# Performance work log

Hardware: AMD Instinct MI355X
Metric: run time of the kernel (lower is better)

## Reference

```python
import jax, jax.numpy as jnp
import numpy as np

G, B, K, D = 16384, 4, 2, 64
NEG = -1e30


def _mlp3(x, w1, b1, w2, b2, w3, b3):
    # MLP: linear->relu x3 (BatchNorm defined but unused in original forward)
    h = jax.nn.relu(x @ w1 + b1)
    h = jax.nn.relu(h @ w2 + b2)
    return jax.nn.relu(h @ w3 + b3)


def setup_inputs() -> dict:
    key = jax.random.key(0)
    ks = jax.random.split(key, 32)

    def lin(k, fan_in, fan_out):
        k1, k2 = jax.random.split(k)
        s = 1.0 / np.sqrt(fan_in)
        w = jax.random.uniform(k1, (fan_in, fan_out), jnp.float32, -s, s)
        b = jax.random.uniform(k2, (fan_out,), jnp.float32, -s, s)
        return w, b

    inp = {}
    inp['ap_feat'] = jax.random.normal(ks[0], (G, B, 1), jnp.float32)
    inp['e_feat'] = jax.random.normal(ks[1], (G, B, K, 2), jnp.float32)
    inp['w_pre_ap'], inp['b_pre_ap'] = lin(ks[2], 1, D)
    inp['w_pre_edge'], inp['b_pre_edge'] = lin(ks[3], 2, D)
    # mlp_update_5 (AP-side neighbor messages), _6 (UE-side), _7 (edge update)
    inp['w5_1'], inp['b5_1'] = lin(ks[4], 2 * D, D)
    inp['w5_2'], inp['b5_2'] = lin(ks[5], D, D)
    inp['w5_3'], inp['b5_3'] = lin(ks[6], D, D)
    inp['w6_1'], inp['b6_1'] = lin(ks[7], 2 * D, D)
    inp['w6_2'], inp['b6_2'] = lin(ks[8], D, D)
    inp['w6_3'], inp['b6_3'] = lin(ks[9], D, D)
    inp['w7_1'], inp['b7_1'] = lin(ks[10], 2 * D, D)
    inp['w7_2'], inp['b7_2'] = lin(ks[11], D, D)
    inp['w7_3'], inp['b7_3'] = lin(ks[12], D, D)
    inp['w_post'], inp['b_post'] = lin(ks[13], D, 2)
    return inp


def _edge_conv(e, a, w5_1, b5_1, w5_2, b5_2, w5_3, b5_3,
               w6_1, b6_1, w6_2, b6_2, w6_3, b6_3,
               w7_1, b7_1, w7_2, b7_2, w7_3, b7_3):
    # e: [G,B,K,D] AP2UE edge hid; a: [G,B,D] AP hid.
    # M1[g,b,j] = mlp5(cat(a[g,b], e[g,b,j])) -- same-AP neighbor edges
    x1 = jnp.concatenate([jnp.broadcast_to(a[:, :, None, :], e.shape), e], axis=-1)  # [G,B,K,2D]
    M1 = _mlp3(x1, w5_1, b5_1, w5_2, b5_2, w5_3, b5_3)  # [G,B,K,D]
    # M2[g,b,bp,k] = mlp6(cat(a[g,b], e[g,bp,k])) -- same-UE neighbor edges
    # (original uses the SRC AP feature here too). Split first linear to
    # avoid materializing the [G,B,B,K,2D] concat.
    h = jax.nn.relu(
        (a @ w6_1[:D])[:, :, None, None, :]
        + (e @ w6_1[D:])[:, None, :, :, :]
        + b6_1)  # [G,B,B,K,D]
    h = jax.nn.relu(h @ w6_2 + b6_2)
    M2 = jax.nn.relu(h @ w6_3 + b6_3)  # [G,B,Bp,K,D]
    # masked max excluding the edge itself
    eyeK = jnp.eye(K, dtype=bool)  # [k, j]
    m1max = jnp.max(jnp.where(eyeK[None, None, :, :, None], NEG,
                              M1[:, :, None, :, :]), axis=3)  # [G,B,K,D]
    eyeB = jnp.eye(B, dtype=bool)  # [b, bp]
    m2max = jnp.max(jnp.where(eyeB[None, :, :, None, None], NEG, M2), axis=2)  # [G,B,K,D]
    agg = jnp.maximum(m1max, m2max)
    # new edge feature: mlp7(cat(agg, e_hid))
    return _mlp3(jnp.concatenate([agg, e], axis=-1),
                 w7_1, b7_1, w7_2, b7_2, w7_3, b7_3)


def reference(ap_feat, e_feat, w_pre_ap, b_pre_ap, w_pre_edge, b_pre_edge,
              w5_1, b5_1, w5_2, b5_2, w5_3, b5_3,
              w6_1, b6_1, w6_2, b6_2, w6_3, b6_3,
              w7_1, b7_1, w7_2, b7_2, w7_3, b7_3,
              w_post, b_post):
    # PreLayer (live branches only: AP nodes and AP2UE edges; APConv/UEConv
    # write node 'new' which is never read, so UE/UE2AP branches are dead).
    a = jax.nn.relu(ap_feat @ w_pre_ap + b_pre_ap)   # [G,B,D]
    e = jax.nn.relu(e_feat @ w_pre_edge + b_pre_edge)  # [G,B,K,D]
    # two UpdateLayers (shared weights: ModuleList([UpdateLayer()]*2) + global MLPs)
    for _ in range(2):
        e = _edge_conv(e, a, w5_1, b5_1, w5_2, b5_2, w5_3, b5_3,
                       w6_1, b6_1, w6_2, b6_2, w6_3, b6_3,
                       w7_1, b7_1, w7_2, b7_2, w7_3, b7_3)
    out = e @ w_post + b_post  # [G,B,K,2]
    r, im = out[..., 0], out[..., 1]
    # norm_func: per-graph [B,K] complex matrix, each row (over K) L2-normalized
    n = jnp.sqrt(jnp.sum(r * r + im * im, axis=-1, keepdims=True))
    return jnp.stack([r / n, im / n], axis=-1)  # [G,B,K,2]
```

## Files before the change

### kernel.cpp

```cpp
#include <hip/hip_runtime.h>


typedef unsigned short u16;
typedef unsigned int   u32;
typedef __attribute__((ext_vector_type(8))) short short8_t;
typedef __attribute__((ext_vector_type(2))) short short2v;
typedef __attribute__((ext_vector_type(4))) float floatx4;

#define OFF_W51 0
#define OFF_W61 8192
#define OFF_W71 16384
#define OFF_W52 24576
#define OFF_W53 28672
#define OFF_W62 32768
#define OFF_W63 36864
#define OFF_W72 40960
#define OFF_W73 45056
#define WS_U16  49152

#define CB51 0
#define CB52 64
#define CB53 128
#define CB61 192
#define CB62 256
#define CB63 320
#define CB71 384
#define CB72 448
#define CB73 512
#define CWPO 576
#define CBPO 704
#define CWPA 768
#define CBPA 832
#define CWPE 896
#define CBPE 1024
#define CSZ  1088

#define PW_U16 3584

struct Params {
  const float *ap, *ef;
  const float *wpa, *bpa, *wpe, *bpe;
  const float *w51, *b51, *w52, *b52, *w53, *b53;
  const float *w61, *b61, *w62, *b62, *w63, *b63;
  const float *w71, *b71, *w72, *b72, *w73, *b73;
  const float *wpost, *bpost;
  float *out;
  int gtot;
};

__device__ __forceinline__ u32 pk2(float a, float b) {
  const u32 ua = __float_as_uint(a) + 0x8000u;
  const u32 ub = __float_as_uint(b) + 0x8000u;
  return __builtin_amdgcn_perm(ub, ua, 0x07060302u);
}
__device__ __forceinline__ float blo(u32 v) { return __uint_as_float(v << 16); }
__device__ __forceinline__ float bhi(u32 v) { return __uint_as_float(v & 0xffff0000u); }
__device__ __forceinline__ u32 pkmax(u32 a, u32 b) {
  const short2v r = __builtin_elementwise_max(__builtin_bit_cast(short2v, a),
                                              __builtin_bit_cast(short2v, b));
  return __builtin_bit_cast(u32, r);
}
__device__ __forceinline__ u32 ror16(u32 x) { return (x >> 16) | (x << 16); }
__device__ __forceinline__ float sel4(int i, float x0, float x1, float x2, float x3) {
  const float lo = (i & 1) ? x1 : x0;
  const float hi = (i & 1) ? x3 : x2;
  return (i & 2) ? hi : lo;
}

__device__ __forceinline__ floatx4 mfma16(short8_t a, short8_t b, floatx4 c) {
  return __builtin_amdgcn_mfma_f32_16x16x32_bf16(a, b, c, 0, 0, 0);
}
__device__ __forceinline__ short8_t ldA(const u16* buf, int l) {
  return *(const short8_t*)(buf + l * 8);
}

template<int TSTRIDE>
__device__ __forceinline__ void layerK64R(floatx4* acc, short8_t a0, short8_t a1,
                                          const u16* B, int l) {
#pragma unroll
  for (int t = 0; t < 4; ++t) {
    const short8_t b0 = *(const short8_t*)(B + (t * TSTRIDE + 0) * 512 + l * 8);
    const short8_t b1 = *(const short8_t*)(B + (t * TSTRIDE + 1) * 512 + l * 8);
    acc[t] = mfma16(a0, b0, acc[t]);
    acc[t] = mfma16(a1, b1, acc[t]);
  }
}

__device__ __forceinline__ void layerK64B(floatx4* acc, short8_t a0, short8_t a1,
                                          const short8_t* Bw) {
#pragma unroll
  for (int t = 0; t < 4; ++t) {
    acc[t] = mfma16(a0, Bw[2 * t + 0], acc[t]);
    acc[t] = mfma16(a1, Bw[2 * t + 1], acc[t]);
  }
}

__device__ __forceinline__ void layerK128R(floatx4* acc, short8_t a0, short8_t a1,
                                           short8_t a2, short8_t a3,
                                           const u16* B, int l) {
  short8_t a[4] = {a0, a1, a2, a3};
#pragma unroll
  for (int t = 0; t < 4; ++t)
#pragma unroll
    for (int h = 0; h < 4; ++h)
      acc[t] = mfma16(a[h], *(const short8_t*)(B + (t * 4 + h) * 512 + l * 8), acc[t]);
}

__device__ __forceinline__ void scatter_relu_bf16(u16* dst, const floatx4* acc, int q, int n) {
#pragma unroll
  for (int t = 0; t < 4; ++t) {
    const int kk = (t & 1) * 2 + (n >> 3);
    u16* base = dst + (t >> 1) * 512 + (n & 7);
    const u32 v01 = pk2(fmaxf(acc[t][0], 0.f), fmaxf(acc[t][1], 0.f));
    const u32 v23 = pk2(fmaxf(acc[t][2], 0.f), fmaxf(acc[t][3], 0.f));
    base[(4 * q + 0 + 16 * kk) * 8] = (u16)v01;
    base[(4 * q + 1 + 16 * kk) * 8] = (u16)(v01 >> 16);
    base[(4 * q + 2 + 16 * kk) * 8] = (u16)v23;
    base[(4 * q + 3 + 16 * kk) * 8] = (u16)(v23 >> 16);
  }
}

__device__ __forceinline__ void scatter_bf16(u16* dst, const floatx4* acc, int q, int n) {
#pragma unroll
  for (int t = 0; t < 4; ++t) {
    const int kk = (t & 1) * 2 + (n >> 3);
    u16* base = dst + (t >> 1) * 512 + (n & 7);
    const u32 v01 = pk2(acc[t][0], acc[t][1]);
    const u32 v23 = pk2(acc[t][2], acc[t][3]);
    base[(4 * q + 0 + 16 * kk) * 8] = (u16)v01;
    base[(4 * q + 1 + 16 * kk) * 8] = (u16)(v01 >> 16);
    base[(4 * q + 2 + 16 * kk) * 8] = (u16)v23;
    base[(4 * q + 3 + 16 * kk) * 8] = (u16)(v23 >> 16);
  }
}

__device__ __forceinline__ void scatter_pk(u16* dst, const u32* src, int q, int n) {
#pragma unroll
  for (int t = 0; t < 4; ++t) {
    const int kk = (t & 1) * 2 + (n >> 3);
    u16* base = dst + (t >> 1) * 512 + (n & 7);
#pragma unroll
    for (int half = 0; half < 2; ++half) {
      const u32 v = src[2 * t + half];
      base[(4 * q + 2 * half + 0 + 16 * kk) * 8] = (u16)v;
      base[(4 * q + 2 * half + 1 + 16 * kk) * 8] = (u16)(v >> 16);
    }
  }
}

__device__ __forceinline__ void scatter_aP(u16* dst, const floatx4* acc, int q, int n,
                                           const float* cb61) {
#pragma unroll
  for (int t = 0; t < 4; ++t) {
    const int kk = (t & 1) * 2 + (n >> 3);
    u16* base = dst + (t >> 1) * 256 + (n & 7);
    const float bv = cb61[16 * t + n];
    const u32 v = pk2(acc[t][0] + bv, acc[t][2] + bv);
    base[(2 * q + 0 + 8 * kk) * 8] = (u16)v;
    base[(2 * q + 1 + 8 * kk) * 8] = (u16)(v >> 16);
  }
}

__device__ __forceinline__ void init_accL(floatx4* acc, const float* cb, int n) {
#pragma unroll
  for (int t = 0; t < 4; ++t) {
    const float b = cb[16 * t + n];
    floatx4 v; v[0] = b; v[1] = b; v[2] = b; v[3] = b;
    acc[t] = v;
  }
}

struct frag2 { short8_t f0, f1; };

__device__ __forceinline__ frag2 make_a(float apv, int q, const float* sc) {
  frag2 r;
#pragma unroll
  for (int h = 0; h < 2; ++h) {
    const int fb = 32 * h + 8 * q;
    const float4 wa0 = *(const float4*)(sc + CWPA + fb);
    const float4 wa1 = *(const float4*)(sc + CWPA + fb + 4);
    const float4 ba0 = *(const float4*)(sc + CBPA + fb);
    const float4 ba1 = *(const float4*)(sc + CBPA + fb + 4);
    uint4 pa;
    pa.x = pk2(fmaxf(fmaf(apv, wa0.x, ba0.x), 0.f), fmaxf(fmaf(apv, wa0.y, ba0.y), 0.f));
    pa.y = pk2(fmaxf(fmaf(apv, wa0.z, ba0.z), 0.f), fmaxf(fmaf(apv, wa0.w, ba0.w), 0.f));
    pa.z = pk2(fmaxf(fmaf(apv, wa1.x, ba1.x), 0.f), fmaxf(fmaf(apv, wa1.y, ba1.y), 0.f));
    pa.w = pk2(fmaxf(fmaf(apv, wa1.z, ba1.z), 0.f), fmaxf(fmaf(apv, wa1.w, ba1.w), 0.f));
    if (h == 0) r.f0 = __builtin_bit_cast(short8_t, pa);
    else        r.f1 = __builtin_bit_cast(short8_t, pa);
  }
  return r;
}

#define NBLK 256
#define NWAVE 8
#define PPW  4

__global__ __launch_bounds__(512)
__attribute__((amdgpu_waves_per_eu(2)))
void hetgnn_mfma(Params p) {
  __shared__ __align__(16) u16   sW[WS_U16];
  __shared__ __align__(16) u16   sAct[NWAVE * PW_U16];
  __shared__ __align__(16) float sConst[CSZ];

  const int tid  = threadIdx.x;
  const int wave = tid >> 6;
  const int l    = tid & 63;
  const int q    = l >> 4;
  const int n    = l & 15;

  {
    const float* mats[9] = {p.w51, p.w61, p.w71, p.w52, p.w53, p.w62, p.w63, p.w72, p.w73};
    for (int i = 0; i < 12; ++i) {
      const int fi = wave * 12 + i;
      const float* W;
      int t, h;
      if (fi < 48) { W = mats[fi >> 4]; const int loc = fi & 15; t = loc >> 2; h = loc & 3; }
      else { const int j = fi - 48; W = mats[3 + (j >> 3)]; const int loc = j & 7; t = loc >> 1; h = loc & 1; }
      const int nn = 16 * t + (l & 15);
      const int k0 = 32 * h + (l >> 4) * 8;
      float w[8];
#pragma unroll
      for (int j = 0; j < 8; ++j) w[j] = W[(k0 + j) * 64 + nn];
      uint4 o;
      o.x = pk2(w[0], w[1]); o.y = pk2(w[2], w[3]);
      o.z = pk2(w[4], w[5]); o.w = pk2(w[6], w[7]);
      *(uint4*)(sW + fi * 512 + l * 8) = o;
    }
  }
  if (tid < 64) {
    sConst[CB51 + tid] = p.b51[tid];
    sConst[CB52 + tid] = p.b52[tid];
    sConst[CB53 + tid] = p.b53[tid];
    sConst[CB61 + tid] = p.b61[tid];
    sConst[CB62 + tid] = p.b62[tid];
    sConst[CB63 + tid] = p.b63[tid];
    sConst[CB71 + tid] = p.b71[tid];
    sConst[CB72 + tid] = p.b72[tid];
    sConst[CB73 + tid] = p.b73[tid];
    sConst[CWPA + tid] = p.wpa[tid];
    sConst[CBPA + tid] = p.bpa[tid];
    sConst[CBPE + tid] = p.bpe[tid];
  }
  if (tid < 128) {
    sConst[CWPO + tid] = p.wpost[tid];
    sConst[CWPE + tid] = p.wpe[tid];
  }
  if (tid < 2) sConst[CBPO + tid] = p.bpost[tid];
  __syncthreads();

  short8_t bw62[8], bw63[8];
#pragma unroll
  for (int f = 0; f < 8; ++f) {
    bw62[f] = *(const short8_t*)(sW + OFF_W62 + f * 512 + l * 8);
    bw63[f] = *(const short8_t*)(sW + OFF_W63 + f * 512 + l * 8);
  }

  u16* Eb  = sAct + wave * PW_U16;
  u16* T1  = Eb + 1024;
  u16* eP  = Eb + 2048;
  u16* aPb = Eb + 3072;

  const int wslot = blockIdx.x * NWAVE + wave;

  for (int pi = 0; pi < PPW; ++pi) {
    const int g0 = (wslot * PPW + pi) * 2;
    if (g0 + 2 > p.gtot) break;

    const float apv = p.ap[(g0 + (n >> 3)) * 4 + ((n >> 1) & 3)];
    const frag2 A = make_a(apv, q, sConst);
    short8_t e0, e1;
    {
      const float f0 = p.ef[(g0 + (n >> 3)) * 16 + (n & 7) * 2];
      const float f1 = p.ef[(g0 + (n >> 3)) * 16 + (n & 7) * 2 + 1];
#pragma unroll
      for (int h = 0; h < 2; ++h) {
        const int fb = 32 * h + 8 * q;
        const float4 w00 = *(const float4*)(sConst + CWPE + fb);
        const float4 w01 = *(const float4*)(sConst + CWPE + fb + 4);
        const float4 w10 = *(const float4*)(sConst + CWPE + 64 + fb);
        const float4 w11 = *(const float4*)(sConst + CWPE + 64 + fb + 4);
        const float4 be0 = *(const float4*)(sConst + CBPE + fb);
        const float4 be1 = *(const float4*)(sConst + CBPE + fb + 4);
        uint4 pe;
        pe.x = pk2(fmaxf(fmaf(f0, w00.x, fmaf(f1, w10.x, be0.x)), 0.f),
                   fmaxf(fmaf(f0, w00.y, fmaf(f1, w10.y, be0.y)), 0.f));
        pe.y = pk2(fmaxf(fmaf(f0, w00.z, fmaf(f1, w10.z, be0.z)), 0.f),
                   fmaxf(fmaf(f0, w00.w, fmaf(f1, w10.w, be0.w)), 0.f));
        pe.z = pk2(fmaxf(fmaf(f0, w01.x, fmaf(f1, w11.x, be1.x)), 0.f),
                   fmaxf(fmaf(f0, w01.y, fmaf(f1, w11.y, be1.y)), 0.f));
        pe.w = pk2(fmaxf(fmaf(f0, w01.z, fmaf(f1, w11.z, be1.z)), 0.f),
                   fmaxf(fmaf(f0, w01.w, fmaf(f1, w11.w, be1.w)), 0.f));
        if (h == 0) e0 = __builtin_bit_cast(short8_t, pe);
        else        e1 = __builtin_bit_cast(short8_t, pe);
      }
    }

    {
      floatx4 accA[4];
#pragma unroll
      for (int t = 0; t < 4; ++t) { accA[t][0] = 0.f; accA[t][1] = 0.f; accA[t][2] = 0.f; accA[t][3] = 0.f; }
      layerK64R<4>(accA, A.f0, A.f1, sW + OFF_W61, l);
      scatter_aP(aPb, accA, q, n, sConst + CB61);
    }

#pragma unroll 1
    for (int it = 0; it < 2; ++it) {
      if (it == 1) { e0 = ldA(Eb, l); e1 = ldA(Eb + 512, l); }

      u32 m1p[8];
      {
        floatx4 acc[4]; init_accL(acc, sConst + CB51, n);
        layerK128R(acc, A.f0, A.f1, e0, e1, sW + OFF_W51, l);
        scatter_relu_bf16(T1, acc, q, n);
        floatx4 acc2[4]; init_accL(acc2, sConst + CB52, n);
        layerK64R<2>(acc2, ldA(T1, l), ldA(T1 + 512, l), sW + OFF_W52, l);
        scatter_relu_bf16(T1, acc2, q, n);
        floatx4 acc3[4]; init_accL(acc3, sConst + CB53, n);
        layerK64R<2>(acc3, ldA(T1, l), ldA(T1 + 512, l), sW + OFF_W53, l);
#pragma unroll
        for (int t = 0; t < 4; ++t) {
          m1p[2 * t + 0] = pk2(acc3[t][0], acc3[t][1]);
          m1p[2 * t + 1] = pk2(acc3[t][2], acc3[t][3]);
        }
      }

      u32 m2p[8];
      {
        floatx4 accE[4];
#pragma unroll
        for (int t = 0; t < 4; ++t) { accE[t][0] = 0.f; accE[t][1] = 0.f; accE[t][2] = 0.f; accE[t][3] = 0.f; }
        layerK64R<4>(accE, e0, e1, sW + OFF_W61 + 2 * 512, l);
        scatter_bf16(eP, accE, q, n);

        const int d = n >> 1;
        const int b_ln = (n >> 1) & 3;
#pragma unroll
        for (int j = 0; j < 3; ++j) {
          const int bp = (j >= b_ln) ? (j + 1) : j;
          const int re = (n & 8) + bp * 2 + (n & 1);
          short8_t h0, h1;
#pragma unroll
          for (int h = 0; h < 2; ++h) {
            const uint4 av = *(const uint4*)(aPb + h * 256 + (d + 8 * q) * 8);
            const uint4 ev = *(const uint4*)(eP + h * 512 + (re + 16 * q) * 8);
            uint4 ph;
            ph.x = pk2(fmaxf(blo(av.x) + blo(ev.x), 0.f),
                       fmaxf(bhi(av.x) + bhi(ev.x), 0.f));
            ph.y = pk2(fmaxf(blo(av.y) + blo(ev.y), 0.f),
                       fmaxf(bhi(av.y) + bhi(ev.y), 0.f));
            ph.z = pk2(fmaxf(blo(av.z) + blo(ev.z), 0.f),
                       fmaxf(bhi(av.z) + bhi(ev.z), 0.f));
            ph.w = pk2(fmaxf(blo(av.w) + blo(ev.w), 0.f),
                       fmaxf(bhi(av.w) + bhi(ev.w), 0.f));
            if (h == 0) h0 = __builtin_bit_cast(short8_t, ph);
            else        h1 = __builtin_bit_cast(short8_t, ph);
          }
          floatx4 acc2[4]; init_accL(acc2, sConst + CB62, n);
          layerK64B(acc2, h0, h1, bw62);
          scatter_relu_bf16(T1, acc2, q, n);
          floatx4 acc3[4]; init_accL(acc3, sConst + CB63, n);
          layerK64B(acc3, ldA(T1, l), ldA(T1 + 512, l), bw63);
#pragma unroll
          for (int t = 0; t < 4; ++t) {
#pragma unroll
            for (int h = 0; h < 2; ++h) {
              const u32 cand = pk2(acc3[t][2 * h], acc3[t][2 * h + 1]);
              m2p[2 * t + h] = (j == 0) ? cand : pkmax(m2p[2 * t + h], cand);
            }
          }
        }
      }

      {
        u32 agp[8];
#pragma unroll
        for (int i = 0; i < 8; ++i)
          agp[i] = pkmax(pkmax(ror16(m1p[i]), m2p[i]), 0u);
        scatter_pk(T1, agp, q, n);
        floatx4 acc[4]; init_accL(acc, sConst + CB71, n);
        layerK128R(acc, ldA(T1, l), ldA(T1 + 512, l), e0, e1, sW + OFF_W71, l);
        scatter_relu_bf16(T1, acc, q, n);
        floatx4 acc2[4]; init_accL(acc2, sConst + CB72, n);
        layerK64R<2>(acc2, ldA(T1, l), ldA(T1 + 512, l), sW + OFF_W72, l);
        scatter_relu_bf16(T1, acc2, q, n);
        floatx4 acc3[4]; init_accL(acc3, sConst + CB73, n);
        layerK64R<2>(acc3, ldA(T1, l), ldA(T1 + 512, l), sW + OFF_W73, l);

        if (it == 0) {
          scatter_relu_bf16(Eb, acc3, q, n);
        } else {
          float prr[4] = {0.f, 0.f, 0.f, 0.f}, pii[4] = {0.f, 0.f, 0.f, 0.f};
#pragma unroll
          for (int t = 0; t < 4; ++t) {
            const float wr = sConst[CWPO + (16 * t + n) * 2];
            const float wi = sConst[CWPO + (16 * t + n) * 2 + 1];
#pragma unroll
            for (int r = 0; r < 4; ++r) {
              const float e = fmaxf(acc3[t][r], 0.f);
              prr[r] = fmaf(e, wr, prr[r]);
              pii[r] = fmaf(e, wi, pii[r]);
            }
          }
          const float bpR = sConst[CBPO], bpI = sConst[CBPO + 1];
#pragma unroll
          for (int r = 0; r < 4; ++r) {
#pragma unroll
            for (int off = 1; off < 16; off <<= 1) {
              prr[r] += __shfl_xor(prr[r], off, 16);
              pii[r] += __shfl_xor(pii[r], off, 16);
            }
            prr[r] += bpR;
            pii[r] += bpI;
          }
          const int r = n >> 1, c = n & 1, rp = r ^ 1;
          const float pr_r  = sel4(r,  prr[0], prr[1], prr[2], prr[3]);
          const float pi_r  = sel4(r,  pii[0], pii[1], pii[2], pii[3]);
          const float pr_rp = sel4(rp, prr[0], prr[1], prr[2], prr[3]);
          const float pi_rp = sel4(rp, pii[0], pii[1], pii[2], pii[3]);
          const float num = c ? pi_r : pr_r;
          const float n2  = pr_r * pr_r + pi_r * pi_r + pr_rp * pr_rp + pi_rp * pi_rp;
          if (n < 8) p.out[g0 * 16 + (4 * q + r) * 2 + c] = num / sqrtf(n2);
        }
      }
    }
  }
}

extern "C" void kernel_launch(void* const* d_in, const int* in_sizes, int n_in,
                              void* d_out, int out_size, void* d_ws, size_t ws_size,
                              hipStream_t stream) {
  Params p;
  p.ap    = (const float*)d_in[0];
  p.ef    = (const float*)d_in[1];
  p.wpa   = (const float*)d_in[2];  p.bpa   = (const float*)d_in[3];
  p.wpe   = (const float*)d_in[4];  p.bpe   = (const float*)d_in[5];
  p.w51   = (const float*)d_in[6];  p.b51   = (const float*)d_in[7];
  p.w52   = (const float*)d_in[8];  p.b52   = (const float*)d_in[9];
  p.w53   = (const float*)d_in[10]; p.b53   = (const float*)d_in[11];
  p.w61   = (const float*)d_in[12]; p.b61   = (const float*)d_in[13];
  p.w62   = (const float*)d_in[14]; p.b62   = (const float*)d_in[15];
  p.w63   = (const float*)d_in[16]; p.b63   = (const float*)d_in[17];
  p.w71   = (const float*)d_in[18]; p.b71   = (const float*)d_in[19];
  p.w72   = (const float*)d_in[20]; p.b72   = (const float*)d_in[21];
  p.w73   = (const float*)d_in[22]; p.b73   = (const float*)d_in[23];
  p.wpost = (const float*)d_in[24]; p.bpost = (const float*)d_in[25];
  p.out   = (float*)d_out;
  p.gtot  = in_sizes[0] / 4;

  hipLaunchKernelGGL(hetgnn_mfma, dim3(NBLK), dim3(512), 0, stream, p);
}
```

Measured before the change: 166.0 us.

## Double waves per block by shrinking per-wave LDS and register footprint

Raises each block from 8 to 16 waves (1024 threads, waves_per_eu 4) and halves the pairs handled per wave. To make room, the four per-wave activation buffers are collapsed into one shared scratch plus the aP buffer. The W62 weight fragments are now built straight from global memory into registers, while W63 is no longer held in registers and is read from LDS instead. The M2 hidden fragments are precomputed for all three neighbours before the MLP passes, since the scratch buffer that held eP is later overwritten. This trades extra LDS reads and register pressure limits for higher occupancy and latency hiding.

```diff
diff --git a/kernel.cpp b/kernel.cpp
--- a/kernel.cpp
+++ b/kernel.cpp
@@ -12,11 +12,10 @@
 #define OFF_W71 16384
 #define OFF_W52 24576
 #define OFF_W53 28672
-#define OFF_W62 32768
-#define OFF_W63 36864
-#define OFF_W72 40960
-#define OFF_W73 45056
-#define WS_U16  49152
+#define OFF_W63 32768
+#define OFF_W72 36864
+#define OFF_W73 40960
+#define WS_U16  45056
 
 #define CB51 0
 #define CB52 64
@@ -35,7 +34,7 @@
 #define CBPE 1024
 #define CSZ  1088
 
-#define PW_U16 3584
+#define PW_U16 1536
 
 struct Params {
   const float *ap, *ef;
@@ -193,11 +192,11 @@
 }
 
 #define NBLK 256
-#define NWAVE 8
-#define PPW  4
-
-__global__ __launch_bounds__(512)
-__attribute__((amdgpu_waves_per_eu(2)))
+#define NWAVE 16
+#define PPW  2
+
+__global__ __launch_bounds__(1024)
+__attribute__((amdgpu_waves_per_eu(4)))
 void hetgnn_mfma(Params p) {
   __shared__ __align__(16) u16   sW[WS_U16];
   __shared__ __align__(16) u16   sAct[NWAVE * PW_U16];
@@ -210,15 +209,14 @@
   const int n    = l & 15;
 
   {
-    const float* mats[9] = {p.w51, p.w61, p.w71, p.w52, p.w53, p.w62, p.w63, p.w72, p.w73};
-    for (int i = 0; i < 12; ++i) {
-      const int fi = wave * 12 + i;
+    const float* mats[8] = {p.w51, p.w61, p.w71, p.w52, p.w53, p.w63, p.w72, p.w73};
+    for (int fi = wave; fi < 88; fi += NWAVE) {
       const float* W;
       int t, h;
       if (fi < 48) { W = mats[fi >> 4]; const int loc = fi & 15; t = loc >> 2; h = loc & 3; }
       else { const int j = fi - 48; W = mats[3 + (j >> 3)]; const int loc = j & 7; t = loc >> 1; h = loc & 1; }
-      const int nn = 16 * t + (l & 15);
-      const int k0 = 32 * h + (l >> 4) * 8;
+      const int nn = 16 * t + n;
+      const int k0 = 32 * h + q * 8;
       float w[8];
 #pragma unroll
       for (int j = 0; j < 8; ++j) w[j] = W[(k0 + j) * 64 + nn];
@@ -249,17 +247,22 @@
   if (tid < 2) sConst[CBPO + tid] = p.bpost[tid];
   __syncthreads();
 
-  short8_t bw62[8], bw63[8];
+  short8_t bw62[8];
 #pragma unroll
   for (int f = 0; f < 8; ++f) {
-    bw62[f] = *(const short8_t*)(sW + OFF_W62 + f * 512 + l * 8);
-    bw63[f] = *(const short8_t*)(sW + OFF_W63 + f * 512 + l * 8);
-  }
-
-  u16* Eb  = sAct + wave * PW_U16;
-  u16* T1  = Eb + 1024;
-  u16* eP  = Eb + 2048;
-  u16* aPb = Eb + 3072;
+    const int nn = 16 * (f >> 1) + n;
+    const int k0 = 32 * (f & 1) + q * 8;
+    float w[8];
+#pragma unroll
+    for (int j = 0; j < 8; ++j) w[j] = p.w62[(k0 + j) * 64 + nn];
+    uint4 o;
+    o.x = pk2(w[0], w[1]); o.y = pk2(w[2], w[3]);
+    o.z = pk2(w[4], w[5]); o.w = pk2(w[6], w[7]);
+    bw62[f] = __builtin_bit_cast(short8_t, o);
+  }
+
+  u16* BUF = sAct + wave * PW_U16;
+  u16* aPb = BUF + 1024;
 
   const int wslot = blockIdx.x * NWAVE + wave;
 
@@ -306,18 +309,18 @@
 
 #pragma unroll 1
     for (int it = 0; it < 2; ++it) {
-      if (it == 1) { e0 = ldA(Eb, l); e1 = ldA(Eb + 512, l); }
+      if (it == 1) { e0 = ldA(BUF, l); e1 = ldA(BUF + 512, l); }
 
       u32 m1p[8];
       {
         floatx4 acc[4]; init_accL(acc, sConst + CB51, n);
         layerK128R(acc, A.f0, A.f1, e0, e1, sW + OFF_W51, l);
-        scatter_relu_bf16(T1, acc, q, n);
+        scatter_relu_bf16(BUF, acc, q, n);
         floatx4 acc2[4]; init_accL(acc2, sConst + CB52, n);
-        layerK64R<2>(acc2, ldA(T1, l), ldA(T1 + 512, l), sW + OFF_W52, l);
-        scatter_relu_bf16(T1, acc2, q, n);
+        layerK64R<2>(acc2, ldA(BUF, l), ldA(BUF + 512, l), sW + OFF_W52, l);
+        scatter_relu_bf16(BUF, acc2, q, n);
         floatx4 acc3[4]; init_accL(acc3, sConst + CB53, n);
-        layerK64R<2>(acc3, ldA(T1, l), ldA(T1 + 512, l), sW + OFF_W53, l);
+        layerK64R<2>(acc3, ldA(BUF, l), ldA(BUF + 512, l), sW + OFF_W53, l);
 #pragma unroll
         for (int t = 0; t < 4; ++t) {
           m1p[2 * t + 0] = pk2(acc3[t][0], acc3[t][1]);
@@ -331,19 +334,19 @@
 #pragma unroll
         for (int t = 0; t < 4; ++t) { accE[t][0] = 0.f; accE[t][1] = 0.f; accE[t][2] = 0.f; accE[t][3] = 0.f; }
         layerK64R<4>(accE, e0, e1, sW + OFF_W61 + 2 * 512, l);
-        scatter_bf16(eP, accE, q, n);
+        scatter_bf16(BUF, accE, q, n);
 
         const int d = n >> 1;
-        const int b_ln = (n >> 1) & 3;
+        const int b_ln = d & 3;
+        short8_t hf0[3], hf1[3];
 #pragma unroll
         for (int j = 0; j < 3; ++j) {
           const int bp = (j >= b_ln) ? (j + 1) : j;
           const int re = (n & 8) + bp * 2 + (n & 1);
-          short8_t h0, h1;
 #pragma unroll
           for (int h = 0; h < 2; ++h) {
             const uint4 av = *(const uint4*)(aPb + h * 256 + (d + 8 * q) * 8);
-            const uint4 ev = *(const uint4*)(eP + h * 512 + (re + 16 * q) * 8);
+            const uint4 ev = *(const uint4*)(BUF + h * 512 + (re + 16 * q) * 8);
             uint4 ph;
             ph.x = pk2(fmaxf(blo(av.x) + blo(ev.x), 0.f),
                        fmaxf(bhi(av.x) + bhi(ev.x), 0.f));
@@ -353,14 +356,17 @@
                        fmaxf(bhi(av.z) + bhi(ev.z), 0.f));
             ph.w = pk2(fmaxf(blo(av.w) + blo(ev.w), 0.f),
                        fmaxf(bhi(av.w) + bhi(ev.w), 0.f));
-            if (h == 0) h0 = __builtin_bit_cast(short8_t, ph);
-            else        h1 = __builtin_bit_cast(short8_t, ph);
+            if (h == 0) hf0[j] = __builtin_bit_cast(short8_t, ph);
+            else        hf1[j] = __builtin_bit_cast(short8_t, ph);
           }
+        }
+#pragma unroll
+        for (int j = 0; j < 3; ++j) {
           floatx4 acc2[4]; init_accL(acc2, sConst + CB62, n);
-          layerK64B(acc2, h0, h1, bw62);
-          scatter_relu_bf16(T1, acc2, q, n);
+          layerK64B(acc2, hf0[j], hf1[j], bw62);
+          scatter_relu_bf16(BUF, acc2, q, n);
           floatx4 acc3[4]; init_accL(acc3, sConst + CB63, n);
-          layerK64B(acc3, ldA(T1, l), ldA(T1 + 512, l), bw63);
+          layerK64R<2>(acc3, ldA(BUF, l), ldA(BUF + 512, l), sW + OFF_W63, l);
 #pragma unroll
           for (int t = 0; t < 4; ++t) {
 #pragma unroll
@@ -377,18 +383,18 @@
 #pragma unroll
         for (int i = 0; i < 8; ++i)
           agp[i] = pkmax(pkmax(ror16(m1p[i]), m2p[i]), 0u);
-        scatter_pk(T1, agp, q, n);
+        scatter_pk(BUF, agp, q, n);
         floatx4 acc[4]; init_accL(acc, sConst + CB71, n);
-        layerK128R(acc, ldA(T1, l), ldA(T1 + 512, l), e0, e1, sW + OFF_W71, l);
-        scatter_relu_bf16(T1, acc, q, n);
+        layerK128R(acc, ldA(BUF, l), ldA(BUF + 512, l), e0, e1, sW + OFF_W71, l);
+        scatter_relu_bf16(BUF, acc, q, n);
         floatx4 acc2[4]; init_accL(acc2, sConst + CB72, n);
-        layerK64R<2>(acc2, ldA(T1, l), ldA(T1 + 512, l), sW + OFF_W72, l);
-        scatter_relu_bf16(T1, acc2, q, n);
+        layerK64R<2>(acc2, ldA(BUF, l), ldA(BUF + 512, l), sW + OFF_W72, l);
+        scatter_relu_bf16(BUF, acc2, q, n);
         floatx4 acc3[4]; init_accL(acc3, sConst + CB73, n);
-        layerK64R<2>(acc3, ldA(T1, l), ldA(T1 + 512, l), sW + OFF_W73, l);
+        layerK64R<2>(acc3, ldA(BUF, l), ldA(BUF + 512, l), sW + OFF_W73, l);
 
         if (it == 0) {
-          scatter_relu_bf16(Eb, acc3, q, n);
+          scatter_relu_bf16(BUF, acc3, q, n);
         } else {
           float prr[4] = {0.f, 0.f, 0.f, 0.f}, pii[4] = {0.f, 0.f, 0.f, 0.f};
 #pragma unroll
@@ -448,5 +454,5 @@
   p.out   = (float*)d_out;
   p.gtot  = in_sizes[0] / 4;
 
-  hipLaunchKernelGGL(hetgnn_mfma, dim3(NBLK), dim3(512), 0, stream, p);
-}
+  hipLaunchKernelGGL(hetgnn_mfma, dim3(NBLK), dim3(1024), 0, stream, p);
+}
```

New measurement: 194.2 us. +17.0%, slower.
